# Optimization experiments

Hardware: AMD Instinct MI355X
Metric: run time of the kernel (lower is better)

The kernel has to match this reference:

```python
import jax, jax.numpy as jnp
import numpy as np

KERNEL_SIZE = 5


def _blur_kernel(log_lengthscale, k):
    # Gaussian-like kernel over squared-squared distance, normalized to sum 1.
    ls = jnp.exp(log_lengthscale)
    coords = jnp.arange(k, dtype=log_lengthscale.dtype) - k // 2
    xs = coords[:, None]
    ys = coords[None, :]
    d2 = (xs ** 2 + ys ** 2) ** 2
    unscaled = jnp.exp(-d2 / (2.0 * ls))
    return unscaled / unscaled.sum()  # [k, k]


def setup_inputs() -> dict:
    key = jax.random.key(0)
    x = jax.random.normal(key, (32, 128, 128, 128), dtype=jnp.float32)
    log_lengthscale = jnp.asarray(-1.0, dtype=jnp.float32)  # nn.Parameter(-ones(()))
    return {"x": x, "log_lengthscale": log_lengthscale}


def reference(x, log_lengthscale):
    k = KERNEL_SIZE
    shape = x.shape
    C = shape[-3]
    xb = x.reshape((-1,) + shape[-3:])  # [B, C, H, W]
    w2d = _blur_kernel(log_lengthscale, k)
    # eye-masked CxCxkxk conv is mathematically a depthwise conv with the same
    # kernel on every channel: weight [C, 1, k, k], feature_group_count=C.
    weight = jnp.broadcast_to(w2d[None, None, :, :], (C, 1, k, k))
    pad = k // 2
    out = jax.lax.conv_general_dilated(
        xb, weight,
        window_strides=(1, 1),
        padding=[(pad, pad), (pad, pad)],
        feature_group_count=C,
        dimension_numbers=("NCHW", "OIHW", "NCHW"),
    )
    return out.reshape(shape)
```

## Files before the change

### kernel.cpp

```cpp
#include <hip/hip_runtime.h>

#define H 128
#define W 128
#define RR 32
#define GPI (H / RR)

__global__ __launch_bounds__(256, 4) void blur5x5_kernel(
        const float* __restrict__ x,
        const float* __restrict__ p_lls,
        float* __restrict__ out,
        int n_groups) {

    float ls2 = 2.0f * expf(p_lls[0]);
    float w[5][5];
    float wsum = 0.0f;
    #pragma unroll
    for (int i = 0; i < 5; ++i) {
        #pragma unroll
        for (int j = 0; j < 5; ++j) {
            float cx = (float)(i - 2);
            float cy = (float)(j - 2);
            float q  = cx * cx + cy * cy;
            float u  = expf(-(q * q) / ls2);
            w[i][j] = u;
            wsum += u;
        }
    }
    float winv = 1.0f / wsum;
    #pragma unroll
    for (int i = 0; i < 5; ++i) {
        #pragma unroll
        for (int j = 0; j < 5; ++j) w[i][j] *= winv;
    }

    int gib   = threadIdx.x >> 5;
    int wl    = threadIdx.x & 31;
    int group = blockIdx.x * (blockDim.x >> 5) + gib;
    if (group >= n_groups) return;
    int img = group / GPI;
    int rg  = group - img * GPI;
    int r0  = rg * RR;

    const float* ib = x   + (size_t)img * (H * W);
    float*       ob = out + (size_t)img * (H * W);
    int xc = wl * 4;

    float acc[5][4];
    #pragma unroll
    for (int d = 0; d < 5; ++d) {
        #pragma unroll
        for (int p = 0; p < 4; ++p) acc[d][p] = 0.0f;
    }

    #pragma unroll 6
    for (int i = 0; i < RR + 4; ++i) {
        int yi = r0 - 2 + i;
        float4 v = make_float4(0.0f, 0.0f, 0.0f, 0.0f);
        if (yi >= 0 && yi < H)
            v = *reinterpret_cast<const float4*>(ib + yi * W + xc);

        float l2 = __shfl_up(v.z, 1, 32);
        float l3 = __shfl_up(v.w, 1, 32);
        float r4 = __shfl_down(v.x, 1, 32);
        float r5 = __shfl_down(v.y, 1, 32);
        if (wl == 0)  { l2 = 0.0f; l3 = 0.0f; }
        if (wl == 31) { r4 = 0.0f; r5 = 0.0f; }
        float win[8] = { l2, l3, v.x, v.y, v.z, v.w, r4, r5 };

        #pragma unroll
        for (int d = 0; d < 5; ++d) {
            const int t = 4 - d;
            #pragma unroll
            for (int p = 0; p < 4; ++p) {
                float s = acc[d][p];
                #pragma unroll
                for (int dx = 0; dx < 5; ++dx)
                    s = fmaf(w[t][dx], win[p + dx], s);
                acc[d][p] = s;
            }
        }

        if (i >= 4) {
            float4 o = make_float4(acc[0][0], acc[0][1], acc[0][2], acc[0][3]);
            *reinterpret_cast<float4*>(ob + (size_t)(r0 + i - 4) * W + xc) = o;
        }

        #pragma unroll
        for (int d = 0; d < 4; ++d) {
            #pragma unroll
            for (int p = 0; p < 4; ++p) acc[d][p] = acc[d + 1][p];
        }
        #pragma unroll
        for (int p = 0; p < 4; ++p) acc[4][p] = 0.0f;
    }
}

extern "C" void kernel_launch(void* const* d_in, const int* in_sizes, int n_in,
                              void* d_out, int out_size, void* d_ws, size_t ws_size,
                              hipStream_t stream) {
    (void)n_in; (void)out_size; (void)d_ws; (void)ws_size;
    const float* x   = (const float*)d_in[0];
    const float* lls = (const float*)d_in[1];
    float* out = (float*)d_out;

    int n_img    = in_sizes[0] / (H * W);
    int n_groups = n_img * GPI;
    int threads  = 256;
    int gpb      = threads / 32;
    int blocks   = (n_groups + gpb - 1) / gpb;

    blur5x5_kernel<<<blocks, threads, 0, stream>>>(x, lls, out, n_groups);
}
```

Before: 447.6 us.

## Exploit kernel symmetry to cut FMAs and use nontemporal output stores

Uses the radial symmetry of the 5x5 blur weights. Each input row gets three horizontal partial sums (pairing symmetric taps), and these are reused across the five vertical accumulators, which cuts arithmetic per row from 100 FMAs to a few dozen ops. Only six unique weights are computed with expf instead of 25. Output rows are written with nontemporal stores to reduce cache pollution, and the loop is unrolled 4 instead of 6. The summation order changes, so results can differ slightly in floating point. The kernel is likely memory bound, so the gain from fewer ops may be small.

```diff
diff --git a/kernel.cpp b/kernel.cpp
--- a/kernel.cpp
+++ b/kernel.cpp
@@ -5,59 +5,52 @@
 #define RR 32
 #define GPI (H / RR)
 
+typedef float f32x4 __attribute__((ext_vector_type(4)));
+
 __global__ __launch_bounds__(256, 4) void blur5x5_kernel(
         const float* __restrict__ x,
         const float* __restrict__ p_lls,
         float* __restrict__ out,
         int n_groups) {
 
-    float ls2 = 2.0f * expf(p_lls[0]);
-    float w[5][5];
-    float wsum = 0.0f;
-    #pragma unroll
-    for (int i = 0; i < 5; ++i) {
-        #pragma unroll
-        for (int j = 0; j < 5; ++j) {
-            float cx = (float)(i - 2);
-            float cy = (float)(j - 2);
-            float q  = cx * cx + cy * cy;
-            float u  = expf(-(q * q) / ls2);
-            w[i][j] = u;
-            wsum += u;
-        }
-    }
-    float winv = 1.0f / wsum;
-    #pragma unroll
-    for (int i = 0; i < 5; ++i) {
-        #pragma unroll
-        for (int j = 0; j < 5; ++j) w[i][j] *= winv;
-    }
+    float ils = -1.0f / (2.0f * expf(p_lls[0]));
+    float u1 = expf(1.0f  * ils);
+    float u2 = expf(4.0f  * ils);
+    float u4 = expf(16.0f * ils);
+    float u5 = expf(25.0f * ils);
+    float u8 = expf(64.0f * ils);
+    float inv = 1.0f / (1.0f + 4.0f * (u1 + u2 + u4 + u8) + 8.0f * u5);
+    float wa = inv;
+    float wb = u1 * inv;
+    float wc = u2 * inv;
+    float wd = u4 * inv;
+    float we = u5 * inv;
+    float wf = u8 * inv;
 
     int gib   = threadIdx.x >> 5;
     int wl    = threadIdx.x & 31;
     int group = blockIdx.x * (blockDim.x >> 5) + gib;
     if (group >= n_groups) return;
-    int img = group / GPI;
-    int rg  = group - img * GPI;
+    int img = group >> 2;
+    int rg  = group & (GPI - 1);
     int r0  = rg * RR;
 
-    const float* ib = x   + (size_t)img * (H * W);
-    float*       ob = out + (size_t)img * (H * W);
-    int xc = wl * 4;
+    const float* ib = x   + (size_t)img * (H * W) + wl * 4;
+    float*       ob = out + (size_t)img * (H * W) + wl * 4;
 
-    float acc[5][4];
+    float acc0[4], acc1[4], acc2[4], acc3[4], acc4[4];
     #pragma unroll
-    for (int d = 0; d < 5; ++d) {
-        #pragma unroll
-        for (int p = 0; p < 4; ++p) acc[d][p] = 0.0f;
+    for (int p = 0; p < 4; ++p) {
+        acc0[p] = 0.0f; acc1[p] = 0.0f; acc2[p] = 0.0f;
+        acc3[p] = 0.0f; acc4[p] = 0.0f;
     }
 
-    #pragma unroll 6
+    #pragma unroll 4
     for (int i = 0; i < RR + 4; ++i) {
         int yi = r0 - 2 + i;
-        float4 v = make_float4(0.0f, 0.0f, 0.0f, 0.0f);
+        f32x4 v = (f32x4)(0.0f);
         if (yi >= 0 && yi < H)
-            v = *reinterpret_cast<const float4*>(ib + yi * W + xc);
+            v = *reinterpret_cast<const f32x4*>(ib + yi * W);
 
         float l2 = __shfl_up(v.z, 1, 32);
         float l3 = __shfl_up(v.w, 1, 32);
@@ -65,33 +58,35 @@
         float r5 = __shfl_down(v.y, 1, 32);
         if (wl == 0)  { l2 = 0.0f; l3 = 0.0f; }
         if (wl == 31) { r4 = 0.0f; r5 = 0.0f; }
-        float win[8] = { l2, l3, v.x, v.y, v.z, v.w, r4, r5 };
+        float e[8] = { l2, l3, v.x, v.y, v.z, v.w, r4, r5 };
 
         #pragma unroll
-        for (int d = 0; d < 5; ++d) {
-            const int t = 4 - d;
-            #pragma unroll
-            for (int p = 0; p < 4; ++p) {
-                float s = acc[d][p];
-                #pragma unroll
-                for (int dx = 0; dx < 5; ++dx)
-                    s = fmaf(w[t][dx], win[p + dx], s);
-                acc[d][p] = s;
-            }
+        for (int p = 0; p < 4; ++p) {
+            float sA = e[p]     + e[p + 4];
+            float sB = e[p + 1] + e[p + 3];
+            float c  = e[p + 2];
+            float h0 = fmaf(wf, sA, fmaf(we, sB, wd * c));
+            float h1 = fmaf(we, sA, fmaf(wc, sB, wb * c));
+            float h2 = fmaf(wd, sA, fmaf(wb, sB, wa * c));
+            acc0[p] += h0;
+            acc1[p] += h1;
+            acc2[p] += h2;
+            acc3[p] += h1;
+            acc4[p] += h0;
         }
 
         if (i >= 4) {
-            float4 o = make_float4(acc[0][0], acc[0][1], acc[0][2], acc[0][3]);
-            *reinterpret_cast<float4*>(ob + (size_t)(r0 + i - 4) * W + xc) = o;
+            f32x4 o = { acc0[0], acc0[1], acc0[2], acc0[3] };
+            __builtin_nontemporal_store(
+                o, reinterpret_cast<f32x4*>(ob + (size_t)(r0 + i - 4) * W));
         }
 
         #pragma unroll
-        for (int d = 0; d < 4; ++d) {
-            #pragma unroll
-            for (int p = 0; p < 4; ++p) acc[d][p] = acc[d + 1][p];
+        for (int p = 0; p < 4; ++p) {
+            acc0[p] = acc1[p]; acc1[p] = acc2[p];
+            acc2[p] = acc3[p]; acc3[p] = acc4[p];
+            acc4[p] = 0.0f;
         }
-        #pragma unroll
-        for (int p = 0; p < 4; ++p) acc[4][p] = 0.0f;
     }
 }
 
```

Result: no change. 451.7 us (+0.9%).
